# Optimization experiments

Hardware: AMD Instinct MI355X
Metric: run time of the kernel (lower is better)

Reference implementation:

```python
import jax, jax.numpy as jnp
import numpy as np

# --- module hyperparameters (from init_kwargs) ---
N_IN = 8192      # n_inputs
N_COL = 4096     # n_columns (64*64, perfect square for 2D topology)
B = 256          # batch of SDRs (forward_batch interface)
K = 40
DELTA_PLUS = 0.015
DELTA_MINUS = 0.000134
DELTA_MINUS_FLOOR = 2.68e-05
GAMMA_FLOOR = 0.2
CONNECTED_PERM = 0.2
POTENTIAL_PCT = 0.5
NEWBORN_STEPS = 1000
TAU_DECAY = 5000
SIGMA = 0.8
BETA = 3.0


def setup_inputs() -> dict:
    key = jax.random.key(0)
    k1, k2, k3 = jax.random.split(key, 3)
    x = (jax.random.uniform(k1, (B, N_IN)) < 0.05).astype(jnp.float32)
    # potential pool: exactly n_potential random inputs per column (argsort of noise)
    n_potential = max(1, int(POTENTIAL_PCT * N_IN))
    noise = jax.random.uniform(k2, (N_COL, N_IN))
    top_idx = jnp.argsort(noise, axis=1)[:, :n_potential]
    potential_mask = jnp.zeros((N_COL, N_IN), dtype=bool).at[
        jnp.arange(N_COL)[:, None], top_idx].set(True)
    # permanences uniform in [0.1, 0.3] inside the pool, 0 elsewhere
    permanences = jnp.where(
        potential_mask,
        jax.random.uniform(k3, (N_COL, N_IN), minval=0.1, maxval=0.3),
        0.0).astype(jnp.float32)
    # 2D grid topology -> Gaussian neighbor boost weights, row-normalized
    side = int(round(np.sqrt(N_COL)))
    ii, jj = jnp.meshgrid(jnp.arange(side, dtype=jnp.float32),
                          jnp.arange(side, dtype=jnp.float32), indexing='ij')
    coords = jnp.stack([ii.ravel(), jj.ravel()], axis=-1)  # (N_COL, 2)
    dist = jnp.linalg.norm(coords[None, :, :] - coords[:, None, :], axis=-1)
    w = jnp.exp(-0.5 * (dist / SIGMA) ** 2)
    boost_weights = w / w.sum(axis=-1, keepdims=True)
    return {"x": x, "permanences": permanences, "potential_mask": potential_mask,
            "boost_weights": boost_weights, "k": K, "t_step": 2500}


def _gamma(t_step):
    t = jnp.asarray(t_step, jnp.float32)
    frac = jnp.clip((t - NEWBORN_STEPS) / max(float(TAU_DECAY), 1.0), 0.0, 1.0)
    decay = GAMMA_FLOOR + (1.0 - GAMMA_FLOOR) * (1.0 - frac)
    return jnp.where(t < NEWBORN_STEPS, jnp.float32(1.0), decay)


def reference(x, permanences, potential_mask, boost_weights, k, t_step):
    gamma = _gamma(t_step)
    # connected synapses: inside potential pool AND permanence >= threshold
    connected = jnp.where(potential_mask & (permanences >= CONNECTED_PERM),
                          jnp.float32(1.0), jnp.float32(0.0))
    overlap = x @ connected.T                                  # (B, N_COL)
    # homeostatic boost: b_i = 1 + gamma*(exp(beta*(mu_neighbors - d_i)) - 1)
    duty_cycle = jnp.full((N_COL,), K / N_COL, jnp.float32)
    mu = boost_weights @ duty_cycle                            # (N_COL,)
    boost = 1.0 + gamma * (jnp.exp(BETA * (mu - duty_cycle)) - 1.0)
    boosted = overlap * boost[None, :]                         # (B, N_COL)
    # exact top-k winner-take-all
    _, active_idx = jax.lax.top_k(boosted, k)                  # (B, k)
    # batched hebbian update: potentiate active-column synapses on active bits,
    # depress on inactive bits, gated by the potential pool
    dm_eff = DELTA_MINUS_FLOOR + (DELTA_MINUS - DELTA_MINUS_FLOOR) * gamma
    active = jnp.zeros((x.shape[0], N_COL), x.dtype).at[
        jnp.arange(x.shape[0])[:, None], active_idx].set(1.0)  # (B, N_COL)
    x_bin = (x > 0).astype(x.dtype)
    S = active.T @ x_bin                                       # (N_COL, N_IN): co-activity counts
    count = active.sum(axis=0)                                 # (N_COL,): times each column won
    dP = potential_mask.astype(x.dtype) * (
        (DELTA_PLUS + dm_eff) * S - dm_eff * count[:, None])
    new_permanences = jnp.clip(permanences + dP, 0.0, 1.0)
    return boosted, active_idx, new_permanences
```

## Files before the change

### kernel.cpp

```cpp
#include <hip/hip_runtime.h>
#include <stdint.h>

#define BATCH 256
#define NIN 8192
#define NCOL 4096
#define NWORDS 128
#define NBINS 1024
#define MAXCAND 1024

__device__ __forceinline__ float gamma_dev(int t_step) {
    float t = (float)t_step;
    float frac = (t - 1000.0f) / 5000.0f;
    frac = fminf(fmaxf(frac, 0.0f), 1.0f);
    float decay = 0.2f + 0.8f * (1.0f - frac);
    return (t < 1000.0f) ? 1.0f : decay;
}

__global__ void pack_kernel(const float* __restrict__ perm,
                            const float* __restrict__ x,
                            unsigned long long* __restrict__ conn_p,
                            unsigned long long* __restrict__ x_perm,
                            unsigned long long* __restrict__ x_lin,
                            int* __restrict__ count) {
    int blk = blockIdx.x;
    int lane = threadIdx.x & 63;
    int wv = threadIdx.x >> 6;
    if (blk < NCOL) {
        int col = blk;
        if (threadIdx.x == 0) count[col] = 0;
        const float4* row4 = (const float4*)(perm + (size_t)col * NIN);
#pragma unroll
        for (int chunk = wv; chunk < 32; chunk += 4) {
            float4 f = row4[chunk * 64 + lane];
            unsigned long long b0 = __ballot(f.x >= 0.2f);
            unsigned long long b1 = __ballot(f.y >= 0.2f);
            unsigned long long b2 = __ballot(f.z >= 0.2f);
            unsigned long long b3 = __ballot(f.w >= 0.2f);
            unsigned long long w = (lane == 0) ? b0 : (lane == 1) ? b1
                                 : (lane == 2) ? b2 : b3;
            if (lane < 4) conn_p[(chunk * 4 + lane) * NCOL + col] = w;
        }
    } else {
        int b = blk - NCOL;
        const float4* row4 = (const float4*)(x + (size_t)b * NIN);
#pragma unroll
        for (int chunk = wv; chunk < 32; chunk += 4) {
            float4 f = row4[chunk * 64 + lane];
            unsigned long long b0 = __ballot(f.x != 0.0f);
            unsigned long long b1 = __ballot(f.y != 0.0f);
            unsigned long long b2 = __ballot(f.z != 0.0f);
            unsigned long long b3 = __ballot(f.w != 0.0f);
            unsigned long long w = (lane == 0) ? b0 : (lane == 1) ? b1
                                 : (lane == 2) ? b2 : b3;
            if (lane < 4) x_perm[b * NWORDS + chunk * 4 + lane] = w;
        }
        for (int w = wv; w < NWORDS; w += 4) {
            float v = x[b * NIN + w * 64 + lane];
            unsigned long long m = __ballot(v != 0.0f);
            if (lane == 0) x_lin[b * NWORDS + w] = m;
        }
    }
}

__global__ void overlap_kernel(const unsigned long long* __restrict__ x_perm,
                               const unsigned long long* __restrict__ conn_p,
                               float* __restrict__ boosted_out) {
    int ctile = blockIdx.x, btile = blockIdx.y;
    int tid = threadIdx.x;
    int c = ctile * 256 + tid;
    __shared__ unsigned long long xs[8][NWORDS];
    for (int idx = tid; idx < 8 * NWORDS; idx += 256) {
        int r = idx >> 7, w = idx & (NWORDS - 1);
        xs[r][w] = x_perm[(btile * 8 + r) * NWORDS + w];
    }
    __syncthreads();
    unsigned int acc[8];
#pragma unroll
    for (int bb = 0; bb < 8; ++bb) acc[bb] = 0;
    for (int w = 0; w < NWORDS; ++w) {
        unsigned long long cw = conn_p[w * NCOL + c];
#pragma unroll
        for (int bb = 0; bb < 8; ++bb) acc[bb] += __popcll(xs[bb][w] & cw);
    }
    for (int bb = 0; bb < 8; ++bb)
        boosted_out[(btile * 8 + bb) * NCOL + c] = (float)acc[bb];
}

__global__ void topk_kernel(const float* __restrict__ boosted, float* __restrict__ aidx_out,
                            int k, int* __restrict__ count, int* __restrict__ winners) {
    int b = blockIdx.x, tid = threadIdx.x;
    int wv = tid >> 6;
    __shared__ unsigned short vs[NCOL];
    __shared__ int hist[4][NBINS];
    __shared__ int cand[MAXCAND];
    __shared__ int sT, sM;
    for (int i = tid; i < 4 * NBINS; i += 256) hist[i >> 10][i & (NBINS - 1)] = 0;
    if (tid == 0) sM = 0;
    __syncthreads();
    const float4* row4 = (const float4*)(boosted + b * NCOL);
#pragma unroll
    for (int q = 0; q < 4; ++q) {
        int i4 = tid + 256 * q;
        float4 f = row4[i4];
        int c0 = i4 * 4;
        int v0 = (int)f.x, v1 = (int)f.y, v2 = (int)f.z, v3 = (int)f.w;
        v0 = v0 < 0 ? 0 : (v0 > NBINS - 1 ? NBINS - 1 : v0);
        v1 = v1 < 0 ? 0 : (v1 > NBINS - 1 ? NBINS - 1 : v1);
        v2 = v2 < 0 ? 0 : (v2 > NBINS - 1 ? NBINS - 1 : v2);
        v3 = v3 < 0 ? 0 : (v3 > NBINS - 1 ? NBINS - 1 : v3);
        vs[c0] = (unsigned short)v0; vs[c0 + 1] = (unsigned short)v1;
        vs[c0 + 2] = (unsigned short)v2; vs[c0 + 3] = (unsigned short)v3;
        atomicAdd(&hist[wv][v0], 1); atomicAdd(&hist[wv][v1], 1);
        atomicAdd(&hist[wv][v2], 1); atomicAdd(&hist[wv][v3], 1);
    }
    __syncthreads();
    for (int j = tid; j < NBINS; j += 256)
        hist[0][j] += hist[1][j] + hist[2][j] + hist[3][j];
    __syncthreads();
    if (tid < 64) {
        int part = 0;
#pragma unroll
        for (int i = 0; i < 16; ++i) part += hist[0][tid * 16 + i];
        int suf = part;
#pragma unroll
        for (int d = 1; d < 64; d <<= 1) {
            int o = __shfl_down(suf, d, 64);
            if (tid + d < 64) suf += o;
        }
        int above = suf - part;
        if (above < k && suf >= k) {
            int run = above;
            for (int i = 15; i >= 0; --i) {
                int h = hist[0][tid * 16 + i];
                if (run + h >= k) { sT = tid * 16 + i; break; }
                run += h;
            }
        }
    }
    __syncthreads();
    int T = sT;
    for (int c = tid; c < NCOL; c += 256) {
        int v = vs[c];
        if (v >= T) {
            int slot = atomicAdd(&sM, 1);
            if (slot < MAXCAND) cand[slot] = (v << 12) | (NCOL - 1 - c);
        }
    }
    __syncthreads();
    int m = sM; if (m > MAXCAND) m = MAXCAND;
    for (int i = tid; i < m; i += 256) {
        int key = cand[i];
        int r = 0;
        for (int j = 0; j < m; ++j) r += (cand[j] > key);
        if (r < k) {
            int c = (NCOL - 1) - (key & 0xFFF);
            aidx_out[b * k + r] = (float)c;
            int slot = atomicAdd(&count[c], 1);
            winners[c * BATCH + slot] = b;
        }
    }
}

__global__ void update_kernel(const float* __restrict__ perm,
                              const unsigned long long* __restrict__ x_lin,
                              const int* __restrict__ count, const int* __restrict__ winners,
                              const int* __restrict__ t_step,
                              float* __restrict__ perm_out) {
    int col = blockIdx.x;
    int tid = threadIdx.x;
    int cnt = count[col];
    __shared__ int wl[BATCH];
    for (int j = tid; j < cnt; j += 256) wl[j] = winners[col * BATCH + j];
    __syncthreads();
    float g = gamma_dev(t_step[0]);
    float dm = 2.68e-05f + (0.000134f - 2.68e-05f) * g;
    float a = 0.015f + dm;
    float cf = (float)cnt;
    const float4* p4 = (const float4*)(perm + (size_t)col * NIN);
    float4* o4 = (float4*)(perm_out + (size_t)col * NIN);
    for (int jj = 0; jj < 8; ++jj) {
        int idx4 = tid + 256 * jj;
        int i0 = idx4 * 4;
        float4 p = p4[idx4];
        int wi = i0 >> 6, sh = i0 & 63;
        int S0 = 0, S1 = 0, S2 = 0, S3 = 0;
        for (int j = 0; j < cnt; ++j) {
            unsigned long long xw = x_lin[wl[j] * NWORDS + wi];
            unsigned int nib = (unsigned int)((xw >> sh) & 0xFULL);
            S0 += nib & 1; S1 += (nib >> 1) & 1; S2 += (nib >> 2) & 1; S3 += (nib >> 3) & 1;
        }
        float4 r;
        r.x = fminf(fmaxf(p.x + ((p.x > 0.0f) ? (a * (float)S0 - dm * cf) : 0.0f), 0.0f), 1.0f);
        r.y = fminf(fmaxf(p.y + ((p.y > 0.0f) ? (a * (float)S1 - dm * cf) : 0.0f), 0.0f), 1.0f);
        r.z = fminf(fmaxf(p.z + ((p.z > 0.0f) ? (a * (float)S2 - dm * cf) : 0.0f), 0.0f), 1.0f);
        r.w = fminf(fmaxf(p.w + ((p.w > 0.0f) ? (a * (float)S3 - dm * cf) : 0.0f), 0.0f), 1.0f);
        o4[idx4] = r;
    }
}

extern "C" void kernel_launch(void* const* d_in, const int* in_sizes, int n_in,
                              void* d_out, int out_size, void* d_ws, size_t ws_size,
                              hipStream_t stream) {
    const float* x    = (const float*)d_in[0];
    const float* perm = (const float*)d_in[1];
    const int* t_step = (const int*)d_in[5];
    float* out = (float*)d_out;

    int k = (out_size - BATCH * NCOL - NCOL * NIN) / BATCH;
    if (k < 1) k = 1;
    if (k > BATCH) k = BATCH;

    char* ws = (char*)d_ws;
    unsigned long long* x_lin  = (unsigned long long*)(ws + 0);
    unsigned long long* conn_p = (unsigned long long*)(ws + 262144);
    unsigned long long* x_perm = (unsigned long long*)(ws + 4456448);
    int* count   = (int*)(ws + 4718592);
    int* winners = (int*)(ws + 4734976);

    float* boosted_out = out;
    float* aidx_out = out + BATCH * NCOL;
    float* perm_out = out + BATCH * NCOL + BATCH * k;

    pack_kernel<<<NCOL + BATCH, 256, 0, stream>>>(perm, x, conn_p, x_perm, x_lin, count);
    overlap_kernel<<<dim3(16, 32), 256, 0, stream>>>(x_perm, conn_p, boosted_out);
    topk_kernel<<<BATCH, 256, 0, stream>>>(boosted_out, aidx_out, k, count, winners);
    update_kernel<<<NCOL, 256, 0, stream>>>(perm, x_lin, count, winners, t_step, perm_out);
}
```

Baseline: 398.9 us.

## Coalesce connected-bit packing via shared staging and transpose packed inputs

The pack kernel now handles 8 columns per block, stages their bitmasks in shared memory, and writes conn_p with coalesced 8-wide stores instead of scattered single-word stores. Packed input bits are stored word-major (transposed), so the overlap kernel reads them straight from global memory with uniform broadcast loads and no shared-memory staging or barrier. The pack stage gets fewer, heavier blocks, which may reduce parallelism while reading perm. A launch bound is also added to the update kernel.

Result: slower. 414.4 us (+3.9%).

```diff
diff --git a/kernel.cpp b/kernel.cpp
--- a/kernel.cpp
+++ b/kernel.cpp
@@ -19,29 +19,37 @@
 __global__ void pack_kernel(const float* __restrict__ perm,
                             const float* __restrict__ x,
                             unsigned long long* __restrict__ conn_p,
-                            unsigned long long* __restrict__ x_perm,
+                            unsigned long long* __restrict__ x_perm_t,
                             unsigned long long* __restrict__ x_lin,
                             int* __restrict__ count) {
     int blk = blockIdx.x;
     int lane = threadIdx.x & 63;
     int wv = threadIdx.x >> 6;
-    if (blk < NCOL) {
-        int col = blk;
-        if (threadIdx.x == 0) count[col] = 0;
-        const float4* row4 = (const float4*)(perm + (size_t)col * NIN);
-#pragma unroll
-        for (int chunk = wv; chunk < 32; chunk += 4) {
-            float4 f = row4[chunk * 64 + lane];
-            unsigned long long b0 = __ballot(f.x >= 0.2f);
-            unsigned long long b1 = __ballot(f.y >= 0.2f);
-            unsigned long long b2 = __ballot(f.z >= 0.2f);
-            unsigned long long b3 = __ballot(f.w >= 0.2f);
-            unsigned long long w = (lane == 0) ? b0 : (lane == 1) ? b1
-                                 : (lane == 2) ? b2 : b3;
-            if (lane < 4) conn_p[(chunk * 4 + lane) * NCOL + col] = w;
+    if (blk < NCOL / 8) {
+        int col0 = blk * 8;
+        __shared__ unsigned long long cs[8][NWORDS + 1];
+        if (threadIdx.x < 8) count[col0 + threadIdx.x] = 0;
+        for (int cc = 0; cc < 8; ++cc) {
+            const float4* row4 = (const float4*)(perm + (size_t)(col0 + cc) * NIN);
+#pragma unroll
+            for (int chunk = wv; chunk < 32; chunk += 4) {
+                float4 f = row4[chunk * 64 + lane];
+                unsigned long long b0 = __ballot(f.x >= 0.2f);
+                unsigned long long b1 = __ballot(f.y >= 0.2f);
+                unsigned long long b2 = __ballot(f.z >= 0.2f);
+                unsigned long long b3 = __ballot(f.w >= 0.2f);
+                unsigned long long w = (lane == 0) ? b0 : (lane == 1) ? b1
+                                     : (lane == 2) ? b2 : b3;
+                if (lane < 4) cs[cc][chunk * 4 + lane] = w;
+            }
+        }
+        __syncthreads();
+        for (int i = threadIdx.x; i < 8 * NWORDS; i += 256) {
+            int pw = i >> 3, cc = i & 7;
+            conn_p[pw * NCOL + col0 + cc] = cs[cc][pw];
         }
     } else {
-        int b = blk - NCOL;
+        int b = blk - NCOL / 8;
         const float4* row4 = (const float4*)(x + (size_t)b * NIN);
 #pragma unroll
         for (int chunk = wv; chunk < 32; chunk += 4) {
@@ -52,7 +60,7 @@
             unsigned long long b3 = __ballot(f.w != 0.0f);
             unsigned long long w = (lane == 0) ? b0 : (lane == 1) ? b1
                                  : (lane == 2) ? b2 : b3;
-            if (lane < 4) x_perm[b * NWORDS + chunk * 4 + lane] = w;
+            if (lane < 4) x_perm_t[(chunk * 4 + lane) * BATCH + b] = w;
         }
         for (int w = wv; w < NWORDS; w += 4) {
             float v = x[b * NIN + w * 64 + lane];
@@ -62,26 +70,23 @@
     }
 }
 
-__global__ void overlap_kernel(const unsigned long long* __restrict__ x_perm,
+__global__ void overlap_kernel(const unsigned long long* __restrict__ x_perm_t,
                                const unsigned long long* __restrict__ conn_p,
                                float* __restrict__ boosted_out) {
     int ctile = blockIdx.x, btile = blockIdx.y;
-    int tid = threadIdx.x;
-    int c = ctile * 256 + tid;
-    __shared__ unsigned long long xs[8][NWORDS];
-    for (int idx = tid; idx < 8 * NWORDS; idx += 256) {
-        int r = idx >> 7, w = idx & (NWORDS - 1);
-        xs[r][w] = x_perm[(btile * 8 + r) * NWORDS + w];
-    }
-    __syncthreads();
+    int c = ctile * 256 + threadIdx.x;
     unsigned int acc[8];
 #pragma unroll
     for (int bb = 0; bb < 8; ++bb) acc[bb] = 0;
+    const unsigned long long* xb = x_perm_t + btile * 8;
+#pragma unroll 4
     for (int w = 0; w < NWORDS; ++w) {
         unsigned long long cw = conn_p[w * NCOL + c];
-#pragma unroll
-        for (int bb = 0; bb < 8; ++bb) acc[bb] += __popcll(xs[bb][w] & cw);
-    }
+        const unsigned long long* xr = xb + w * BATCH;
+#pragma unroll
+        for (int bb = 0; bb < 8; ++bb) acc[bb] += __popcll(xr[bb] & cw);
+    }
+#pragma unroll
     for (int bb = 0; bb < 8; ++bb)
         boosted_out[(btile * 8 + bb) * NCOL + c] = (float)acc[bb];
 }
@@ -161,7 +166,8 @@
     }
 }
 
-__global__ void update_kernel(const float* __restrict__ perm,
+__global__ void __launch_bounds__(256) update_kernel(
+                              const float* __restrict__ perm,
                               const unsigned long long* __restrict__ x_lin,
                               const int* __restrict__ count, const int* __restrict__ winners,
                               const int* __restrict__ t_step,
@@ -211,9 +217,9 @@
     if (k > BATCH) k = BATCH;
 
     char* ws = (char*)d_ws;
-    unsigned long long* x_lin  = (unsigned long long*)(ws + 0);
-    unsigned long long* conn_p = (unsigned long long*)(ws + 262144);
-    unsigned long long* x_perm = (unsigned long long*)(ws + 4456448);
+    unsigned long long* x_lin    = (unsigned long long*)(ws + 0);
+    unsigned long long* conn_p   = (unsigned long long*)(ws + 262144);
+    unsigned long long* x_perm_t = (unsigned long long*)(ws + 4456448);
     int* count   = (int*)(ws + 4718592);
     int* winners = (int*)(ws + 4734976);
 
@@ -221,8 +227,8 @@
     float* aidx_out = out + BATCH * NCOL;
     float* perm_out = out + BATCH * NCOL + BATCH * k;
 
-    pack_kernel<<<NCOL + BATCH, 256, 0, stream>>>(perm, x, conn_p, x_perm, x_lin, count);
-    overlap_kernel<<<dim3(16, 32), 256, 0, stream>>>(x_perm, conn_p, boosted_out);
+    pack_kernel<<<NCOL / 8 + BATCH, 256, 0, stream>>>(perm, x, conn_p, x_perm_t, x_lin, count);
+    overlap_kernel<<<dim3(16, 32), 256, 0, stream>>>(x_perm_t, conn_p, boosted_out);
     topk_kernel<<<BATCH, 256, 0, stream>>>(boosted_out, aidx_out, k, count, winners);
     update_kernel<<<NCOL, 256, 0, stream>>>(perm, x_lin, count, winners, t_step, perm_out);
 }
```
